# Kernel tuning notes

Hardware: AMD Instinct MI355X
Metric: run time of the kernel (lower is better)

## Reference

```python
import jax, jax.numpy as jnp
import numpy as np

B = 2
ROW, COL = 63, 84          # resolution
ROW_, COL_ = 32, 42        # resolution_
N = ROW * COL              # 5292 kv tokens
N_ = ROW_ * COL_           # 1344 q tokens
IN_DIM, OUT_DIM = 256, 512
KEY_DIM, NUM_HEADS, ATTN_RATIO, STRIDE = 16, 8, 2, 2
D = ATTN_RATIO * KEY_DIM   # 32 (value dim per head)
DH = D * NUM_HEADS         # 256
NH_KD = KEY_DIM * NUM_HEADS  # 128
H_KV = DH + NH_KD          # 384
SCALE = KEY_DIM ** -0.5
EPS = 1e-5


def _build_bias_idxs():
    # replicates the itertools.product double loop, vectorized; ids ordered by
    # first occurrence in row-major scan (same as dict insertion order).
    r_ = np.arange(ROW_); c_ = np.arange(COL_)
    r = np.arange(ROW); c = np.arange(COL)
    off_r = np.abs(r_[:, None] * STRIDE - r[None, :])      # (32, 63)
    off_c = np.abs(c_[:, None] * STRIDE - c[None, :])      # (42, 84)
    keys = (off_r[:, None, :, None] * 1000 + off_c[None, :, None, :]).reshape(-1)
    _, first_idx, inv = np.unique(keys, return_index=True, return_inverse=True)
    order = np.argsort(first_idx)
    rank = np.empty_like(order); rank[order] = np.arange(len(order))
    idxs = rank[inv].reshape(N_, N).astype(np.int32)
    return idxs, len(order)


def setup_inputs() -> dict:
    key = jax.random.key(0)
    ks = jax.random.split(key, 12)
    idxs_np, n_off = _build_bias_idxs()
    inp = {
        "x": jax.random.normal(ks[0], (B, N, IN_DIM), jnp.float32),
        "kv_w": jax.random.normal(ks[1], (H_KV, IN_DIM), jnp.float32) * (IN_DIM ** -0.5),
        "kv_g": jnp.ones((H_KV,), jnp.float32),
        "kv_b": jnp.zeros((H_KV,), jnp.float32),
        "q_w": jax.random.normal(ks[2], (NH_KD, IN_DIM), jnp.float32) * (IN_DIM ** -0.5),
        "q_g": jnp.ones((NH_KD,), jnp.float32),
        "q_b": jnp.zeros((NH_KD,), jnp.float32),
        "proj_w": jax.random.normal(ks[3], (OUT_DIM, DH), jnp.float32) * (DH ** -0.5),
        "proj_g": jnp.ones((OUT_DIM,), jnp.float32),
        "proj_b": jnp.zeros((OUT_DIM,), jnp.float32),
        "bias_table": jax.random.normal(ks[4], (NUM_HEADS, n_off), jnp.float32) * 0.02,
        "bias_idxs": jnp.asarray(idxs_np),
    }
    return inp


def _linear_bn(x, w, g, b):
    # Linear (no bias) followed by BatchNorm1d in training mode (batch stats
    # over flattened (B*N) dim, biased variance).
    y = jnp.einsum("bnc,oc->bno", x, w)
    flat = y.reshape(-1, y.shape[-1])
    mu = flat.mean(0)
    var = flat.var(0)
    return (y - mu) * (g / jnp.sqrt(var + EPS)) + b


def _hardswish(x):
    return x * jnp.clip(x + 3.0, 0.0, 6.0) / 6.0


def reference(x, kv_w, kv_g, kv_b, q_w, q_g, q_b, proj_w, proj_g, proj_b,
              bias_table, bias_idxs):
    Bx = x.shape[0]
    # kv projection -> split k (KEY_DIM) and v (D) per head
    kv = _linear_bn(x, kv_w, kv_g, kv_b).reshape(Bx, N, NUM_HEADS, KEY_DIM + D)
    k = kv[..., :KEY_DIM].transpose(0, 2, 1, 3)   # (B, H, N, key_dim)
    v = kv[..., KEY_DIM:].transpose(0, 2, 1, 3)   # (B, H, N, d)
    # q: spatial subsample then projection
    xs = x.reshape(Bx, ROW, COL, IN_DIM)[:, ::STRIDE, ::STRIDE].reshape(Bx, N_, IN_DIM)
    q = _linear_bn(xs, q_w, q_g, q_b).reshape(Bx, N_, NUM_HEADS, KEY_DIM).transpose(0, 2, 1, 3)
    # gathered relative position bias: (H, N_, N)
    ab = bias_table[:, bias_idxs]
    attn = jnp.einsum("bhqd,bhkd->bhqk", q, k) * SCALE + ab[None]
    attn = jax.nn.softmax(attn, axis=-1)
    out = jnp.einsum("bhqk,bhkd->bhqd", attn, v)       # (B, H, N_, d)
    out = out.transpose(0, 2, 1, 3).reshape(Bx, N_, DH)
    out = _linear_bn(_hardswish(out), proj_w, proj_g, proj_b)
    return out
```

## Files before the change

kernel.cpp:

```cpp
#include <hip/hip_runtime.h>
#include <hip/hip_bf16.h>
#include <math.h>

#define N_K 5292
#define N_KP 5376
#define N_Q 1344
#define NH_KD 128
#define NROWS 21504
#define NSPLIT 8
#define LOG2E 1.4426950408889634f
#define MSTAT 16.0f

typedef float f32x4 __attribute__((ext_vector_type(4)));
typedef short short8 __attribute__((ext_vector_type(8)));

__device__ __forceinline__ float fexp2(float x) {
#if __has_builtin(__builtin_amdgcn_exp2f)
    return __builtin_amdgcn_exp2f(x);
#else
    return exp2f(x);
#endif
}

__device__ __forceinline__ unsigned pk_bf16(float a, float b) {
    union { __hip_bfloat162 h; unsigned u; } c;
    c.h = __float22bfloat162_rn(make_float2(a, b));
    return c.u;
}
__device__ __forceinline__ unsigned short f2bf(float a) {
    return (unsigned short)pk_bf16(a, 0.f);
}

__global__ __launch_bounds__(256) void prep_bf16(
    const float* __restrict__ X, const float* __restrict__ kv_w,
    const float* __restrict__ q_w,
    unsigned short* __restrict__ Xb, float* __restrict__ sums)
{
    int i = blockIdx.x * 256 + threadIdx.x;
    if (i >= 710144) {
        int j = i - 710144;
        float4 z = make_float4(0.f, 0.f, 0.f, 0.f);
        *(float4*)(sums + (size_t)j * 8)     = z;
        *(float4*)(sums + (size_t)j * 8 + 4) = z;
        return;
    }
    const float* src;
    long off;
    if (i < 677376)       { src = X;      off = i; }
    else if (i < 701952)  { src = kv_w;   off = i - 677376; }
    else                  { src = q_w;    off = i - 701952; }
    float4 v = *(const float4*)(src + off * 4);
    *(uint2*)(Xb + (size_t)i * 4) = make_uint2(pk_bf16(v.x, v.y), pk_bf16(v.z, v.w));
}

__device__ __forceinline__ void gemm_body_direct(
    const unsigned short* __restrict__ A, const unsigned short* __restrict__ W,
    long arow, int n0,
    unsigned short (*Bs)[264], f32x4 acc[4])
{
    const int t = threadIdx.x;
    const int lane = t & 63, g = lane >> 4, ln = lane & 15;

    #pragma unroll
    for (int p = 0; p < 8; ++p) {
        int i = p * 256 + t;
        int row = i >> 5, c8 = (i & 31) * 8;
        *(uint4*)&Bs[row][c8] = *(const uint4*)(W + (size_t)(n0 + row) * 256 + c8);
    }
    __syncthreads();

    const unsigned short* aptr =
        (arow >= 0) ? (A + (size_t)arow * 256 + g * 8) : (const unsigned short*)0;

    #pragma unroll
    for (int k0 = 0; k0 < 256; k0 += 32) {
        short8 ah = (short8)0;
        if (aptr) ah = *(const short8*)(aptr + k0);
        #pragma unroll
        for (int nt = 0; nt < 4; ++nt) {
            short8 bh = *(const short8*)&Bs[nt * 16 + ln][k0 + g * 8];
            acc[nt] = __builtin_amdgcn_mfma_f32_16x16x32_bf16(ah, bh, acc[nt], 0, 0, 0);
        }
    }
}

__device__ __forceinline__ void gemm_stats(f32x4 acc[4], float* __restrict__ sums,
                                           int n0, int Ncols, float* scratch)
{
    const int t = threadIdx.x;
    const int w = t >> 6, lane = t & 63, g = lane >> 4, ln = lane & 15;
    float s4[4], q4[4];
    #pragma unroll
    for (int nt = 0; nt < 4; ++nt) {
        float s = acc[nt][0] + acc[nt][1] + acc[nt][2] + acc[nt][3];
        float q = fmaf(acc[nt][0], acc[nt][0], fmaf(acc[nt][1], acc[nt][1],
                  fmaf(acc[nt][2], acc[nt][2], acc[nt][3] * acc[nt][3])));
        s += __shfl_xor(s, 16); s += __shfl_xor(s, 32);
        q += __shfl_xor(q, 16); q += __shfl_xor(q, 32);
        s4[nt] = s; q4[nt] = q;
    }
    __syncthreads();
    float* st_s = scratch;
    float* st_q = scratch + 256;
    if (g == 0) {
        #pragma unroll
        for (int nt = 0; nt < 4; ++nt) {
            st_s[(w * 4 + nt) * 16 + ln] = s4[nt];
            st_q[(w * 4 + nt) * 16 + ln] = q4[nt];
        }
    }
    __syncthreads();
    if (t < 64) {
        int nt = t >> 4, c = t & 15;
        float a = 0.f, b2 = 0.f;
        #pragma unroll
        for (int ww = 0; ww < 4; ++ww) {
            a  += st_s[(ww * 4 + nt) * 16 + c];
            b2 += st_q[(ww * 4 + nt) * 16 + c];
        }
        atomicAdd(&sums[n0 + nt * 16 + c], a);
        atomicAdd(&sums[Ncols + n0 + nt * 16 + c], b2);
    }
}

__global__ __launch_bounds__(256) void gemm_qkv(
    const unsigned short* __restrict__ Xb, const unsigned short* __restrict__ kvWb,
    const unsigned short* __restrict__ qWb,
    const float* __restrict__ bias_table, const int* __restrict__ bias_idxs, int n_off,
    unsigned short* __restrict__ Kp, unsigned short* __restrict__ Vpt,
    float* __restrict__ bt_r,
    float* __restrict__ q_y, float* __restrict__ sums_kv, float* __restrict__ sums_q)
{
    __shared__ unsigned short Bs[64][264];
    const int t = threadIdx.x;
    const int w = t >> 6, lane = t & 63, g = lane >> 4, ln = lane & 15;
    int id = blockIdx.x;

    if (id >= 1104) {
        id -= 1104;
        if (id < 168) {
            int i = id * 256 + t;
            int row = i / 84, j = i - row * 84;
            int slot;
            if (j < 20) {
                int kap = 44 + j;
                slot = 5248 + (((kap & 15) << 2) | (kap >> 4));
            } else {
                slot = 5312 + (j - 20);
            }
            Vpt[(size_t)row * N_KP + slot] = 0;
        } else {
            int i = (id - 168) * 256 + t;
            if (i < 8 * N_K) {
                int h = i / N_K, j = i - h * N_K;
                bt_r[i] = fmaf(bias_table[h * n_off + bias_idxs[j]], LOG2E, -MSTAT);
            }
        }
        return;
    }

    f32x4 acc[4];
    #pragma unroll
    for (int nt = 0; nt < 4; ++nt) acc[nt] = (f32x4){0.f, 0.f, 0.f, 0.f};

    if (id < 1008) {
        const int xcd = id & 7, id8 = id >> 3;
        const int my = xcd + (id8 / 6) * 8, ny = id8 % 6;
        if (my >= 166) return;
        const int m0 = my * 64, n0 = ny * 64;
        int arow0 = m0 + w * 16 + ln;
        long arow = (arow0 < 10584) ? arow0 : -1;
        gemm_body_direct(Xb, kvWb, arow, n0, Bs, acc);

        #pragma unroll
        for (int nt = 0; nt < 4; ++nt) {
            int c = n0 + nt * 16 + ln;
            int hh = c / 48, cc = c - 48 * hh;
            #pragma unroll
            for (int reg = 0; reg < 4; ++reg) {
                int mr = m0 + w * 16 + g * 4 + reg;
                if (mr < 10584) {
                    int bb = mr >= N_K;
                    int key = mr - bb * N_K;
                    unsigned short v16 = f2bf(acc[nt][reg]);
                    if (cc < 16) {
                        Kp[((size_t)(bb * 8 + hh) * N_K + key) * 16 + cc] = v16;
                    } else {
                        int kap = key & 63;
                        int keyp = (key & ~63) | (((kap & 15) << 2) | (kap >> 4));
                        Vpt[((size_t)(bb * 8 + hh) * 32 + cc - 16) * N_KP + keyp] = v16;
                    }
                }
            }
        }
        gemm_stats(acc, sums_kv, n0, 384, (float*)&Bs[0][0]);
    } else {
        id -= 1008;
        const int xcd = id & 7, id8 = id >> 3;
        const int my = xcd + (id8 / 2) * 8, ny = id8 % 2;
        if (my >= 42) return;
        const int m0 = my * 64, n0 = ny * 64;
        int mrow = m0 + w * 16 + ln;
        int bb = mrow / N_Q;
        int i = mrow - bb * N_Q;
        long arow = (long)(bb * N_K + (i / 42) * 168 + (i % 42) * 2);
        gemm_body_direct(Xb, qWb, arow, n0, Bs, acc);

        #pragma unroll
        for (int nt = 0; nt < 4; ++nt)
            #pragma unroll
            for (int reg = 0; reg < 4; ++reg) {
                int mr = m0 + w * 16 + g * 4 + reg;
                q_y[(size_t)mr * 128 + n0 + nt * 16 + ln] = acc[nt][reg];
            }
        gemm_stats(acc, sums_q, n0, 128, (float*)&Bs[0][0]);
    }
}

__global__ __launch_bounds__(256) void gemm_proj(
    const unsigned short* __restrict__ Ap, const unsigned short* __restrict__ Wp,
    float* __restrict__ Y, float* __restrict__ sums)
{
    __shared__ unsigned short Bs[64][264];
    const int t = threadIdx.x;
    const int w = t >> 6, lane = t & 63, g = lane >> 4, ln = lane & 15;
    const int id = blockIdx.x;
    const int xcd = id & 7, id8 = id >> 3;
    const int my = xcd + (id8 / 8) * 8, ny = id8 % 8;
    if (my >= 42) return;
    const int m0 = my * 64, n0 = ny * 64;

    f32x4 acc[4];
    #pragma unroll
    for (int nt = 0; nt < 4; ++nt) acc[nt] = (f32x4){0.f, 0.f, 0.f, 0.f};
    gemm_body_direct(Ap, Wp, (long)(m0 + w * 16 + ln), n0, Bs, acc);

    #pragma unroll
    for (int nt = 0; nt < 4; ++nt)
        #pragma unroll
        for (int reg = 0; reg < 4; ++reg) {
            int mr = m0 + w * 16 + g * 4 + reg;
            Y[(size_t)mr * 512 + n0 + nt * 16 + ln] = acc[nt][reg];
        }
    gemm_stats(acc, sums, n0, 512, (float*)&Bs[0][0]);
}

__global__ __launch_bounds__(256, 4) void attn_mfma(
    const unsigned short* __restrict__ Kp, const unsigned short* __restrict__ Vpt,
    const float* __restrict__ q_y, const float* __restrict__ sums_q,
    const float* __restrict__ q_g, const float* __restrict__ q_b,
    const float* __restrict__ sums_kv, const float* __restrict__ kv_g,
    const float* __restrict__ bt_r,
    float* __restrict__ pl, unsigned short* __restrict__ pacc)
{
    const int id = blockIdx.x;
    const int h = id & 7;
    const int z = (id >> 3) & 15;
    const int qt = id >> 7;
    const int b = z >> 3, ks = z & 7;
    const int t = threadIdx.x;
    const int w = t >> 6, lane = t & 63, g = lane >> 4, ln = lane & 15;

    __shared__ float btm_s[14 * 166];
    __shared__ unsigned short Vt_s[2][32][72];
    __shared__ unsigned short P_s[4][16][72];

    const int q0 = qt * 64;
    const int t0 = (ks * 83) >> 3;
    const int t1 = ((ks + 1) * 83) >> 3;
    const int kstart = t0 * 64;
    const int kend0 = t1 * 64;
    const int kend = kend0 < N_K ? kend0 : N_K;
    const int ntiles = t1 - t0;
    const bool tail = (ks == 7);

    const int kr0 = kstart / 84;
    const int kr1 = (kend - 1) / 84;
    const int rq2min = (q0 / 42) * 2;
    const int rq2max = ((q0 + 63) / 42) * 2;
    const int dmin_r = rq2min - kr1;
    const int rows = (rq2max - kr0) - dmin_r + 1;
    const int nb = rows * 166;
    const unsigned mxb = (unsigned)((nb - 1) * 4);
    {
        const float* src = bt_r + h * N_K;
        for (int j = t; j < nb; j += 256) {
            int rr = j / 166, ii = j - rr * 166;
            int dr = dmin_r + rr; dr = dr < 0 ? -dr : dr;
            int dc = ii - 83; dc = dc < 0 ? -dc : dc;
            btm_s[j] = src[dr * 84 + dc];
        }
    }

    short8 qfrag = (short8)0;
    if (lane < 32) {
        const float invq = 1.f / 2688.f, invk = 1.f / 10584.f;
        const float post = 0.25f * LOG2E;
        const int c0 = h * 16 + g * 8;
        const int ck = h * 48 + g * 8;
        const float* qp = q_y + (size_t)(b * N_Q + q0 + w * 16 + ln) * NH_KD + c0;
        float vv[8];
        #pragma unroll
        for (int j = 0; j < 8; ++j) {
            float mu  = sums_q[c0 + j] * invq;
            float var = fmaf(-mu, mu, sums_q[128 + c0 + j] * invq);
            float s   = q_g[c0 + j] * rsqrtf(var + 1e-5f) * post;
            float vq  = fmaf(qp[j], s, fmaf(-mu, s, q_b[c0 + j] * post));
            float muk = sums_kv[ck + j] * invk;
            float vrk = fmaf(-muk, muk, sums_kv[384 + ck + j] * invk);
            float sk  = kv_g[ck + j] * rsqrtf(vrk + 1e-5f);
            vv[j] = vq * sk;
        }
        union { short8 s; unsigned u[4]; } qf;
        qf.u[0] = pk_bf16(vv[0], vv[1]); qf.u[1] = pk_bf16(vv[2], vv[3]);
        qf.u[2] = pk_bf16(vv[4], vv[5]); qf.u[3] = pk_bf16(vv[6], vv[7]);
        qfrag = qf.s;
    }

    union { short8 s; unsigned u[4]; } onef;
    #pragma unroll
    for (int j = 0; j < 4; ++j) onef.u[j] = 0x3F803F80u;
    const short8 ones = onef.s;

    int baseb[4];
    #pragma unroll
    for (int reg = 0; reg < 4; ++reg) {
        int qg = q0 + w * 16 + g * 4 + reg;
        int rq2 = (qg / 42) * 2;
        int cq2 = (qg % 42) * 2;
        baseb[reg] = ((rq2 - dmin_r) * 166 + cq2 + 83) * 4;
    }
    int offb[4], kcc[4];
    #pragma unroll
    for (int st = 0; st < 4; ++st) {
        int kg = kstart + st * 16 + ln;
        int okr = kg / 84;
        kcc[st] = kg - okr * 84;
        offb[st] = -(okr * 166 + kcc[st]) * 4;
    }

    const char* kb = (const char*)(Kp + (size_t)(b * 8 + h) * N_K * 16)
                   + (size_t)kstart * 32 + ln * 32 + g * 16;
    short8 kC0 = (short8)0, kC1 = (short8)0, kC2 = (short8)0, kC3 = (short8)0;
    short8 kN0 = (short8)0, kN1 = (short8)0, kN2 = (short8)0, kN3 = (short8)0;
    if (lane < 32) {
        kC0 = *(const short8*)(kb);
        kC1 = *(const short8*)(kb + 512);
        kC2 = *(const short8*)(kb + 1024);
        kC3 = *(const short8*)(kb + 1536);
    }
    kb += 2048;

    const int vrow = t >> 3, vc8 = (t & 7) * 8;
    const unsigned short* vptr = Vpt + (size_t)(b * 8 + h) * 32 * N_KP
                                     + (size_t)vrow * N_KP + kstart + vc8;
    uint4 vreg = *(const uint4*)vptr;
    *(uint4*)&Vt_s[0][vrow][vc8] = vreg;
    __syncthreads();

    f32x4 acc0 = {0.f, 0.f, 0.f, 0.f}, acc1 = {0.f, 0.f, 0.f, 0.f};
    f32x4 accL = {0.f, 0.f, 0.f, 0.f};
    int p = 0;

    for (int it = 0; it < ntiles; ++it) {
        const int k0 = kstart + it * 64;
        const bool notlast = (it + 1 < ntiles);
        if (notlast) {
            vreg = *(const uint4*)(vptr + 64);
            if (lane < 32) {
                kN0 = *(const short8*)(kb);
                kN1 = *(const short8*)(kb + 512);
                kN2 = *(const short8*)(kb + 1024);
                kN3 = *(const short8*)(kb + 1536);
            }
        }

        f32x4 sf[4];
        float pv[4][4];
        const bool clampit = tail && (it == ntiles - 1);
        if (!clampit) {
            #pragma unroll
            for (int st = 0; st < 4; ++st) {
                f32x4 cb;
                #pragma unroll
                for (int reg = 0; reg < 4; ++reg) {
                    unsigned ub = (unsigned)(baseb[reg] + offb[st]);
                    cb[reg] = *(const float*)((const char*)btm_s + ub);
                }
                short8 kf = st == 0 ? kC0 : st == 1 ? kC1 : st == 2 ? kC2 : kC3;
                sf[st] = __builtin_amdgcn_mfma_f32_16x16x32_bf16(qfrag, kf, cb, 0, 0, 0);
            }
            #pragma unroll
            for (int st = 0; st < 4; ++st)
                #pragma unroll
                for (int reg = 0; reg < 4; ++reg)
                    pv[st][reg] = fexp2(sf[st][reg]);
        } else {
            #pragma unroll
            for (int st = 0; st < 4; ++st) {
                f32x4 cb;
                #pragma unroll
                for (int reg = 0; reg < 4; ++reg) {
                    unsigned ub = (unsigned)(baseb[reg] + offb[st]);
                    ub = ub > mxb ? mxb : ub;
                    cb[reg] = *(const float*)((const char*)btm_s + ub);
                }
                short8 kf = st == 0 ? kC0 : st == 1 ? kC1 : st == 2 ? kC2 : kC3;
                sf[st] = __builtin_amdgcn_mfma_f32_16x16x32_bf16(qfrag, kf, cb, 0, 0, 0);
            }
            #pragma unroll
            for (int st = 0; st < 4; ++st) {
                bool bad = (k0 + st * 16 + ln) >= N_K;
                #pragma unroll
                for (int reg = 0; reg < 4; ++reg)
                    pv[st][reg] = bad ? 0.f : fexp2(sf[st][reg]);
            }
        }

        #pragma unroll
        for (int reg = 0; reg < 4; ++reg) {
            uint2 pw = make_uint2(pk_bf16(pv[0][reg], pv[1][reg]),
                                  pk_bf16(pv[2][reg], pv[3][reg]));
            *(uint2*)&P_s[w][g * 4 + reg][4 * ln] = pw;
        }
        __asm__ __volatile__("" ::: "memory");

        #pragma unroll
        for (int kt = 0; kt < 2; ++kt) {
            short8 af = *(const short8*)&P_s[w][ln][g * 8 + kt * 32];
            short8 b0 = *(const short8*)&Vt_s[p][ln][g * 8 + kt * 32];
            short8 b1 = *(const short8*)&Vt_s[p][ln + 16][g * 8 + kt * 32];
            acc0 = __builtin_amdgcn_mfma_f32_16x16x32_bf16(af, b0, acc0, 0, 0, 0);
            acc1 = __builtin_amdgcn_mfma_f32_16x16x32_bf16(af, b1, acc1, 0, 0, 0);
            accL = __builtin_amdgcn_mfma_f32_16x16x32_bf16(af, ones, accL, 0, 0, 0);
        }

        if (notlast) {
            int q2 = p ^ 1;
            *(uint4*)&Vt_s[q2][vrow][vc8] = vreg;
            __syncthreads();
            p = q2;
            vptr += 64;
            kb += 2048;
            kC0 = kN0; kC1 = kN1; kC2 = kN2; kC3 = kN3;
        }

        #pragma unroll
        for (int st = 0; st < 4; ++st) {
            kcc[st] += 64;
            if (kcc[st] >= 84) { kcc[st] -= 84; offb[st] -= 584; }
            else offb[st] -= 256;
        }
    }

    const int rbase = (b * 8 + h) * N_Q + q0 + w * 16;
    #pragma unroll
    for (int reg = 0; reg < 4; ++reg) {
        int prow = ks * NROWS + rbase + g * 4 + reg;
        unsigned short* pb = pacc + (size_t)prow * 32;
        pb[ln]      = f2bf(acc0[reg]);
        pb[16 + ln] = f2bf(acc1[reg]);
        if (ln == 0) pl[prow] = accL[reg];
    }
}

__global__ __launch_bounds__(256) void combine_kernel(const float* __restrict__ pl,
                                                      const unsigned short* __restrict__ pacc,
                                                      const float* __restrict__ sums_kv,
                                                      const float* __restrict__ kv_g,
                                                      const float* __restrict__ kv_b,
                                                      unsigned short* __restrict__ attn_o,
                                                      const float* __restrict__ proj_w,
                                                      unsigned short* __restrict__ projWb)
{
    if (blockIdx.x >= 672) {
        int i = (blockIdx.x - 672) * 256 + threadIdx.x;
        float4 v = *(const float4*)(proj_w + (size_t)i * 4);
        *(uint2*)(projWb + (size_t)i * 4) = make_uint2(pk_bf16(v.x, v.y), pk_bf16(v.z, v.w));
        return;
    }
    int idx = blockIdx.x * 256 + threadIdx.x;
    int r = idx >> 3, e4 = (idx & 7) * 4;
    float L = 0.f;
    float vs[4] = {0.f, 0.f, 0.f, 0.f};
    size_t o = (size_t)r * 32 + e4;
    #pragma unroll
    for (int s2 = 0; s2 < NSPLIT; ++s2) {
        L += pl[(size_t)s2 * NROWS + r];
        uint2 pv2 = *(const uint2*)(pacc + (size_t)s2 * NROWS * 32 + o);
        vs[0] += __uint_as_float((pv2.x & 0xffffu) << 16);
        vs[1] += __uint_as_float(pv2.x & 0xffff0000u);
        vs[2] += __uint_as_float((pv2.y & 0xffffu) << 16);
        vs[3] += __uint_as_float(pv2.y & 0xffff0000u);
    }
    float invL = 1.f / L;
    int q = r % N_Q;
    int bh = r / N_Q;
    int hh = bh & 7, b = bh >> 3;
    const int ch = hh * 48 + 16 + e4;
    const float invk = 1.f / 10584.f;
    float hs[4];
    #pragma unroll
    for (int u = 0; u < 4; ++u) {
        float v = vs[u];
        float mu  = sums_kv[ch + u] * invk;
        float var = fmaf(-mu, mu, sums_kv[384 + ch + u] * invk);
        float s   = kv_g[ch + u] * rsqrtf(var + 1e-5f);
        float tt  = fmaf(-mu, s, kv_b[ch + u]);
        v = fmaf(s, v * invL, tt);
        hs[u] = v * fminf(fmaxf(v + 3.f, 0.f), 6.f) * (1.f / 6.f);
    }
    *(uint2*)(attn_o + (size_t)(b * N_Q + q) * 256 + hh * 32 + e4) =
        make_uint2(pk_bf16(hs[0], hs[1]), pk_bf16(hs[2], hs[3]));
}

__global__ __launch_bounds__(256) void norm_apply(
    const float* __restrict__ Y, const float* __restrict__ sums,
    const float* __restrict__ g, const float* __restrict__ bb,
    float* __restrict__ out, int rows, int cols, float inv_rows)
{
    __shared__ float sc_s[64], sh_s[64];
    const int t = threadIdx.x;
    const int c0 = blockIdx.x * 64;
    if (t < 64) {
        int c = c0 + t;
        float mu  = sums[c] * inv_rows;
        float var = fmaf(-mu, mu, sums[cols + c] * inv_rows);
        float s   = g[c] * rsqrtf(var + 1e-5f);
        sc_s[t] = s;
        sh_s[t] = fmaf(-mu, s, bb[c]);
    }
    __syncthreads();
    const int c4 = (t & 15) * 4;
    float4 scv = *(const float4*)&sc_s[c4];
    float4 shv = *(const float4*)&sh_s[c4];
    for (int r = blockIdx.y * 16 + (t >> 4); r < rows; r += gridDim.y * 16) {
        size_t off = (size_t)r * cols + c0 + c4;
        float4 v = *(const float4*)(Y + off);
        v.x = fmaf(v.x, scv.x, shv.x);
        v.y = fmaf(v.y, scv.y, shv.y);
        v.z = fmaf(v.z, scv.z, shv.z);
        v.w = fmaf(v.w, scv.w, shv.w);
        *(float4*)(out + off) = v;
    }
}

extern "C" void kernel_launch(void* const* d_in, const int* in_sizes, int n_in,
                              void* d_out, int out_size, void* d_ws, size_t ws_size,
                              hipStream_t stream) {
    (void)n_in; (void)out_size; (void)ws_size;
    const float* x      = (const float*)d_in[0];
    const float* kv_w   = (const float*)d_in[1];
    const float* kv_g   = (const float*)d_in[2];
    const float* kv_b   = (const float*)d_in[3];
    const float* q_w    = (const float*)d_in[4];
    const float* q_g    = (const float*)d_in[5];
    const float* q_b    = (const float*)d_in[6];
    const float* proj_w = (const float*)d_in[7];
    const float* proj_g = (const float*)d_in[8];
    const float* proj_b = (const float*)d_in[9];
    const float* bias_table = (const float*)d_in[10];
    const int*   bias_idxs  = (const int*)d_in[11];
    const int    n_off = in_sizes[10] / 8;
    float* out = (float*)d_out;

    float* ws = (float*)d_ws;
    float* q_y  = ws;
    unsigned short* pacc_b = (unsigned short*)(q_y + 2688 * 128);
    float* proj_y = (float*)pacc_b;
    float* pl = (float*)(pacc_b + (size_t)NSPLIT * NROWS * 32);
    unsigned short* attn_o = (unsigned short*)(pl + (size_t)NSPLIT * NROWS);
    unsigned short* Kp  = attn_o + 2688 * 256;
    unsigned short* Vpt = Kp + 2 * 8 * N_K * 16;
    float* sums_kv = (float*)(Vpt + 2 * 8 * 32 * N_KP);
    float* sums_q  = sums_kv + 768;
    float* sums_p  = sums_q + 256;
    float* bt_r    = sums_p + 1024;

    unsigned short* Xb     = pacc_b;
    unsigned short* kvWb   = Xb + 10584 * 256;
    unsigned short* qWb    = kvWb + 384 * 256;
    unsigned short* projWb = (unsigned short*)q_y;

    prep_bf16<<<2775, 256, 0, stream>>>(x, kv_w, q_w, Xb, sums_kv);
    gemm_qkv<<<1104 + 168 + 166, 256, 0, stream>>>(Xb, kvWb, qWb, bias_table, bias_idxs,
                                                   n_off, Kp, Vpt, bt_r,
                                                   q_y, sums_kv, sums_q);
    attn_mfma<<<2688, 256, 0, stream>>>(Kp, Vpt, q_y, sums_q, q_g, q_b,
                                        sums_kv, kv_g, bt_r, pl, pacc_b);
    combine_kernel<<<672 + 128, 256, 0, stream>>>(pl, pacc_b, sums_kv, kv_g, kv_b, attn_o,
                                                  proj_w, projWb);
    gemm_proj<<<384, 256, 0, stream>>>(attn_o, projWb, proj_y, sums_p);
    norm_apply<<<dim3(8, 84), 256, 0, stream>>>(proj_y, sums_p, proj_g, proj_b, out,
                                                2688, 512, 1.f / 2688.f);
}
```

Before: 178.9 us.

## Fuse fp32-to-bf16 conversion into GEMM loads and drop the prep kernel

```diff
diff --git a/kernel.cpp b/kernel.cpp
--- a/kernel.cpp
+++ b/kernel.cpp
@@ -31,30 +31,9 @@
     return (unsigned short)pk_bf16(a, 0.f);
 }
 
-__global__ __launch_bounds__(256) void prep_bf16(
-    const float* __restrict__ X, const float* __restrict__ kv_w,
-    const float* __restrict__ q_w,
-    unsigned short* __restrict__ Xb, float* __restrict__ sums)
-{
-    int i = blockIdx.x * 256 + threadIdx.x;
-    if (i >= 710144) {
-        int j = i - 710144;
-        float4 z = make_float4(0.f, 0.f, 0.f, 0.f);
-        *(float4*)(sums + (size_t)j * 8)     = z;
-        *(float4*)(sums + (size_t)j * 8 + 4) = z;
-        return;
-    }
-    const float* src;
-    long off;
-    if (i < 677376)       { src = X;      off = i; }
-    else if (i < 701952)  { src = kv_w;   off = i - 677376; }
-    else                  { src = q_w;    off = i - 701952; }
-    float4 v = *(const float4*)(src + off * 4);
-    *(uint2*)(Xb + (size_t)i * 4) = make_uint2(pk_bf16(v.x, v.y), pk_bf16(v.z, v.w));
-}
-
+template<bool ABF>
 __device__ __forceinline__ void gemm_body_direct(
-    const unsigned short* __restrict__ A, const unsigned short* __restrict__ W,
+    const void* __restrict__ Av, const float* __restrict__ W,
     long arow, int n0,
     unsigned short (*Bs)[264], f32x4 acc[4])
 {
@@ -65,17 +44,30 @@
     for (int p = 0; p < 8; ++p) {
         int i = p * 256 + t;
         int row = i >> 5, c8 = (i & 31) * 8;
-        *(uint4*)&Bs[row][c8] = *(const uint4*)(W + (size_t)(n0 + row) * 256 + c8);
+        const float* wp = W + (size_t)(n0 + row) * 256 + c8;
+        float4 w0 = *(const float4*)(wp);
+        float4 w1 = *(const float4*)(wp + 4);
+        *(uint4*)&Bs[row][c8] = make_uint4(pk_bf16(w0.x, w0.y), pk_bf16(w0.z, w0.w),
+                                           pk_bf16(w1.x, w1.y), pk_bf16(w1.z, w1.w));
     }
     __syncthreads();
-
-    const unsigned short* aptr =
-        (arow >= 0) ? (A + (size_t)arow * 256 + g * 8) : (const unsigned short*)0;
 
     #pragma unroll
     for (int k0 = 0; k0 < 256; k0 += 32) {
         short8 ah = (short8)0;
-        if (aptr) ah = *(const short8*)(aptr + k0);
+        if (arow >= 0) {
+            if (ABF) {
+                ah = *(const short8*)((const unsigned short*)Av + arow * 256 + k0 + g * 8);
+            } else {
+                const float* ap = (const float*)Av + arow * 256 + k0 + g * 8;
+                float4 a0 = *(const float4*)(ap);
+                float4 a1 = *(const float4*)(ap + 4);
+                union { short8 s; unsigned u[4]; } au;
+                au.u[0] = pk_bf16(a0.x, a0.y); au.u[1] = pk_bf16(a0.z, a0.w);
+                au.u[2] = pk_bf16(a1.x, a1.y); au.u[3] = pk_bf16(a1.z, a1.w);
+                ah = au.s;
+            }
+        }
         #pragma unroll
         for (int nt = 0; nt < 4; ++nt) {
             short8 bh = *(const short8*)&Bs[nt * 16 + ln][k0 + g * 8];
@@ -124,8 +116,8 @@
 }
 
 __global__ __launch_bounds__(256) void gemm_qkv(
-    const unsigned short* __restrict__ Xb, const unsigned short* __restrict__ kvWb,
-    const unsigned short* __restrict__ qWb,
+    const float* __restrict__ X, const float* __restrict__ kv_w,
+    const float* __restrict__ q_w,
     const float* __restrict__ bias_table, const int* __restrict__ bias_idxs, int n_off,
     unsigned short* __restrict__ Kp, unsigned short* __restrict__ Vpt,
     float* __restrict__ bt_r,
@@ -170,7 +162,7 @@
         const int m0 = my * 64, n0 = ny * 64;
         int arow0 = m0 + w * 16 + ln;
         long arow = (arow0 < 10584) ? arow0 : -1;
-        gemm_body_direct(Xb, kvWb, arow, n0, Bs, acc);
+        gemm_body_direct<false>(X, kv_w, arow, n0, Bs, acc);
 
         #pragma unroll
         for (int nt = 0; nt < 4; ++nt) {
@@ -204,7 +196,7 @@
         int bb = mrow / N_Q;
         int i = mrow - bb * N_Q;
         long arow = (long)(bb * N_K + (i / 42) * 168 + (i % 42) * 2);
-        gemm_body_direct(Xb, qWb, arow, n0, Bs, acc);
+        gemm_body_direct<false>(X, q_w, arow, n0, Bs, acc);
 
         #pragma unroll
         for (int nt = 0; nt < 4; ++nt)
@@ -218,7 +210,7 @@
 }
 
 __global__ __launch_bounds__(256) void gemm_proj(
-    const unsigned short* __restrict__ Ap, const unsigned short* __restrict__ Wp,
+    const unsigned short* __restrict__ Ap, const float* __restrict__ Wp,
     float* __restrict__ Y, float* __restrict__ sums)
 {
     __shared__ unsigned short Bs[64][264];
@@ -233,7 +225,7 @@
     f32x4 acc[4];
     #pragma unroll
     for (int nt = 0; nt < 4; ++nt) acc[nt] = (f32x4){0.f, 0.f, 0.f, 0.f};
-    gemm_body_direct(Ap, Wp, (long)(m0 + w * 16 + ln), n0, Bs, acc);
+    gemm_body_direct<true>(Ap, Wp, (long)(m0 + w * 16 + ln), n0, Bs, acc);
 
     #pragma unroll
     for (int nt = 0; nt < 4; ++nt)
@@ -283,12 +275,13 @@
     const int nb = rows * 166;
     const unsigned mxb = (unsigned)((nb - 1) * 4);
     {
-        const float* src = bt_r + h * N_K;
-        for (int j = t; j < nb; j += 256) {
-            int rr = j / 166, ii = j - rr * 166;
-            int dr = dmin_r + rr; dr = dr < 0 ? -dr : dr;
-            int dc = ii - 83; dc = dc < 0 ? -dc : dc;
-            btm_s[j] = src[dr * 84 + dc];
+        if (t < 166) {
+            int dc = t - 83; dc = dc < 0 ? -dc : dc;
+            const float* sc = bt_r + h * N_K + dc;
+            for (int rr = 0; rr < rows; ++rr) {
+                int dr = dmin_r + rr; dr = dr < 0 ? -dr : dr;
+                btm_s[rr * 166 + t] = sc[dr * 84];
+            }
         }
     }
 
@@ -469,16 +462,8 @@
                                                       const float* __restrict__ sums_kv,
                                                       const float* __restrict__ kv_g,
                                                       const float* __restrict__ kv_b,
-                                                      unsigned short* __restrict__ attn_o,
-                                                      const float* __restrict__ proj_w,
-                                                      unsigned short* __restrict__ projWb)
-{
-    if (blockIdx.x >= 672) {
-        int i = (blockIdx.x - 672) * 256 + threadIdx.x;
-        float4 v = *(const float4*)(proj_w + (size_t)i * 4);
-        *(uint2*)(projWb + (size_t)i * 4) = make_uint2(pk_bf16(v.x, v.y), pk_bf16(v.z, v.w));
-        return;
-    }
+                                                      unsigned short* __restrict__ attn_o)
+{
     int idx = blockIdx.x * 256 + threadIdx.x;
     int r = idx >> 3, e4 = (idx & 7) * 4;
     float L = 0.f;
@@ -577,20 +562,14 @@
     float* sums_p  = sums_q + 256;
     float* bt_r    = sums_p + 1024;
 
-    unsigned short* Xb     = pacc_b;
-    unsigned short* kvWb   = Xb + 10584 * 256;
-    unsigned short* qWb    = kvWb + 384 * 256;
-    unsigned short* projWb = (unsigned short*)q_y;
-
-    prep_bf16<<<2775, 256, 0, stream>>>(x, kv_w, q_w, Xb, sums_kv);
-    gemm_qkv<<<1104 + 168 + 166, 256, 0, stream>>>(Xb, kvWb, qWb, bias_table, bias_idxs,
+    hipMemsetAsync(sums_kv, 0, 2048 * sizeof(float), stream);
+    gemm_qkv<<<1104 + 168 + 166, 256, 0, stream>>>(x, kv_w, q_w, bias_table, bias_idxs,
                                                    n_off, Kp, Vpt, bt_r,
                                                    q_y, sums_kv, sums_q);
     attn_mfma<<<2688, 256, 0, stream>>>(Kp, Vpt, q_y, sums_q, q_g, q_b,
                                         sums_kv, kv_g, bt_r, pl, pacc_b);
-    combine_kernel<<<672 + 128, 256, 0, stream>>>(pl, pacc_b, sums_kv, kv_g, kv_b, attn_o,
-                                                  proj_w, projWb);
-    gemm_proj<<<384, 256, 0, stream>>>(attn_o, projWb, proj_y, sums_p);
+    combine_kernel<<<672, 256, 0, stream>>>(pl, pacc_b, sums_kv, kv_g, kv_b, attn_o);
+    gemm_proj<<<384, 256, 0, stream>>>(attn_o, proj_w, proj_y, sums_p);
     norm_apply<<<dim3(8, 84), 256, 0, stream>>>(proj_y, sums_p, proj_g, proj_b, out,
                                                 2688, 512, 1.f / 2688.f);
 }
```

Result: no change. 179.5 us (+0.3%).
